# Optimization experiments

Measured on AMD Instinct MI355X. Metric: run time of the kernel, lower is better.

Reference implementation:

```python
import jax, jax.numpy as jnp
import numpy as np

D_MODEL = 1024
NUM_HEADS = 16
ENERGY_SCALE = 0.1
LN_EPS = 1e-5


def layernorm(x, gamma, beta):
    mu = jnp.mean(x, axis=-1, keepdims=True)
    var = jnp.var(x, axis=-1, keepdims=True)
    return (x - mu) * jax.lax.rsqrt(var + LN_EPS) * gamma + beta


def setup_inputs() -> dict:
    key = jax.random.key(0)
    ks = jax.random.split(key, 8)
    B, L, D = 2, 2048, D_MODEL
    s = 0.02
    return {
        "x": jax.random.normal(ks[0], (B, L, D), dtype=jnp.float32),
        "wq": jax.random.normal(ks[1], (D, D), dtype=jnp.float32) * s,
        "wk": jax.random.normal(ks[2], (D, D), dtype=jnp.float32) * s,
        "wv": jax.random.normal(ks[3], (D, D), dtype=jnp.float32) * s,
        "wo_w": jax.random.normal(ks[4], (D, D), dtype=jnp.float32) * s,
        "wo_b": jnp.zeros((D,), dtype=jnp.float32),
        "ep_w": jax.random.normal(ks[5], (D, D), dtype=jnp.float32) * s,
        "ep_b": jnp.zeros((D,), dtype=jnp.float32),
        "en_g": jnp.ones((D,), dtype=jnp.float32),
        "en_b": jnp.zeros((D,), dtype=jnp.float32),
        "ln_g": jnp.ones((D,), dtype=jnp.float32),
        "ln_b": jnp.zeros((D,), dtype=jnp.float32),
    }


def reference(x, wq, wk, wv, wo_w, wo_b, ep_w, ep_b, en_g, en_b, ln_g, ln_b):
    B, L, D = x.shape
    H, dk = NUM_HEADS, D // NUM_HEADS
    # Linear projections (torch convention: y = x @ W^T), split heads -> [B,H,L,dk]
    q = (x @ wq.T).reshape(B, L, H, dk).transpose(0, 2, 1, 3)
    k = (x @ wk.T).reshape(B, L, H, dk).transpose(0, 2, 1, 3)
    v = (x @ wv.T).reshape(B, L, H, dk).transpose(0, 2, 1, 3)
    scores = jnp.einsum("bhld,bhmd->bhlm", q, k) / jnp.sqrt(jnp.float32(dk))
    # Energy bias: ef @ ef^T as a proper GEMM (same math as the broadcast-mul-sum)
    ef = layernorm(x @ ep_w.T + ep_b, en_g, en_b)
    energy_bias = jnp.einsum("bld,bmd->blm", ef, ef)  # [B,L,L]
    scores = scores + ENERGY_SCALE * energy_bias[:, None, :, :]
    attn = jax.nn.softmax(scores, axis=-1)  # dropout is identity in eval mode
    ctx = jnp.einsum("bhlm,bhmd->bhld", attn, v)
    ctx = ctx.transpose(0, 2, 1, 3).reshape(B, L, D)
    out = ctx @ wo_w.T + wo_b
    return layernorm(out + x, ln_g, ln_b), attn
```

## Files before the change

kernel.cpp:

```cpp
#include <hip/hip_runtime.h>
#include <math.h>

#define D_MODEL 1024
#define NUM_HEADS 16
#define DK 64
#define L_SEQ 2048
#define BATCH 2
#define LN_EPS 1e-5f
#define ENERGY_SCALE 0.1f

typedef __attribute__((ext_vector_type(8))) short short8;
typedef __attribute__((ext_vector_type(4))) float f32x4;
typedef __attribute__((address_space(1))) const unsigned int gas_u32;
typedef __attribute__((address_space(3))) unsigned int las_u32;

__device__ __forceinline__ float waveReduceSum(float v) {
#pragma unroll
    for (int off = 32; off > 0; off >>= 1) v += __shfl_xor(v, off, 64);
    return v;
}

__device__ __forceinline__ unsigned short f2bf(float f) {
    unsigned int u = __float_as_uint(f);
    u += 0x7fff + ((u >> 16) & 1);
    return (unsigned short)(u >> 16);
}
__device__ __forceinline__ float bf2f(unsigned short u) {
    return __uint_as_float((unsigned int)u << 16);
}

__global__ __launch_bounds__(256) void cvt6(
    const float* s0, const float* s1, const float* s2,
    const float* s3, const float* s4, const float* s5,
    unsigned short* d0, unsigned short* d1, unsigned short* d2,
    unsigned short* d3, unsigned short* d4, unsigned short* d5,
    long long n0, long long n1, long long n2, long long n3, long long n4, long long n5)
{
    const float* s; unsigned short* d; long long n;
    switch (blockIdx.y) {
        case 0: s = s0; d = d0; n = n0; break;
        case 1: s = s1; d = d1; n = n1; break;
        case 2: s = s2; d = d2; n = n2; break;
        case 3: s = s3; d = d3; n = n3; break;
        case 4: s = s4; d = d4; n = n4; break;
        default: s = s5; d = d5; n = n5; break;
    }
    long long i = ((long long)blockIdx.x * 256 + threadIdx.x) * 4;
    if (i >= n) return;
    float4 v = *(const float4*)(s + i);
    ushort4 o;
    o.x = f2bf(v.x); o.y = f2bf(v.y); o.z = f2bf(v.z); o.w = f2bf(v.w);
    *(ushort4*)(d + i) = o;
}

__global__ __launch_bounds__(256) void gemm_bf16(
    const unsigned short* __restrict__ A, const unsigned short* __restrict__ B,
    const float* __restrict__ bias, float* __restrict__ Cf, unsigned short* __restrict__ Ch,
    int N, int K, long long sA, long long sB, long long sC)
{
    A += (long long)blockIdx.z * sA;
    B += (long long)blockIdx.z * sB;
    __shared__ unsigned short As[128 * 64];
    __shared__ unsigned short Bs[128 * 64];
    const int tid = threadIdx.x;
    const int lane = tid & 63, w = tid >> 6;
    const int quad = lane >> 4, col = lane & 15;
    const int wm = w & 1, wn = w >> 1;
    const int row0 = blockIdx.y * 128, col0 = blockIdx.x * 128;

    const int lr = lane >> 3, lc = lane & 7;
    const int gcs = (lc ^ lr) * 8;

    f32x4 acc[4][4];
#pragma unroll
    for (int mt = 0; mt < 4; mt++)
#pragma unroll
        for (int nt = 0; nt < 4; nt++) acc[mt][nt] = (f32x4){0.f, 0.f, 0.f, 0.f};

    for (int k0 = 0; k0 < K; k0 += 64) {
        __syncthreads();
#pragma unroll
        for (int p = 0; p < 4; p++) {
            const int rb = w * 32 + p * 8;
            __builtin_amdgcn_global_load_lds(
                (gas_u32*)(A + (long long)(row0 + rb + lr) * K + k0 + gcs),
                (las_u32*)(As + rb * 64), 16, 0, 0);
            __builtin_amdgcn_global_load_lds(
                (gas_u32*)(B + (long long)(col0 + rb + lr) * K + k0 + gcs),
                (las_u32*)(Bs + rb * 64), 16, 0, 0);
        }
        __syncthreads();
#pragma unroll
        for (int kc = 0; kc < 2; kc++) {
            const int csw = ((quad + 4 * kc) ^ (col & 7)) * 8;
            short8 af[4], bfr[4];
#pragma unroll
            for (int mt = 0; mt < 4; mt++)
                af[mt] = *(const short8*)(As + (wm * 64 + mt * 16 + col) * 64 + csw);
#pragma unroll
            for (int nt = 0; nt < 4; nt++)
                bfr[nt] = *(const short8*)(Bs + (wn * 64 + nt * 16 + col) * 64 + csw);
#pragma unroll
            for (int mt = 0; mt < 4; mt++)
#pragma unroll
                for (int nt = 0; nt < 4; nt++)
                    acc[mt][nt] = __builtin_amdgcn_mfma_f32_16x16x32_bf16(af[mt], bfr[nt], acc[mt][nt], 0, 0, 0);
        }
    }

#pragma unroll
    for (int mt = 0; mt < 4; mt++)
#pragma unroll
        for (int nt = 0; nt < 4; nt++)
#pragma unroll
            for (int reg = 0; reg < 4; reg++) {
                long long row = row0 + wm * 64 + mt * 16 + quad * 4 + reg;
                int c = col0 + wn * 64 + nt * 16 + col;
                float v = acc[mt][nt][reg];
                if (bias) v += bias[c];
                if (Cf) Cf[blockIdx.z * sC + row * N + c] = v;
                else    Ch[blockIdx.z * sC + row * N + c] = f2bf(v);
            }
}

__global__ __launch_bounds__(256) void proj_gemm(
    const unsigned short* __restrict__ Xh,
    const unsigned short* __restrict__ wqh, const unsigned short* __restrict__ wkh,
    const unsigned short* __restrict__ wvh, const unsigned short* __restrict__ eph,
    const float* __restrict__ ep_b,
    unsigned short* __restrict__ Qh, unsigned short* __restrict__ Kh,
    unsigned short* __restrict__ Vf, float* __restrict__ EP)
{
    const unsigned short* B;
    switch (blockIdx.z) {
        case 0: B = wqh; break;
        case 1: B = wkh; break;
        case 2: B = wvh; break;
        default: B = eph; break;
    }
    __shared__ unsigned short As[128 * 64];
    __shared__ unsigned short Bs[128 * 64];
    const int tid = threadIdx.x;
    const int lane = tid & 63, w = tid >> 6;
    const int quad = lane >> 4, col = lane & 15;
    const int wm = w & 1, wn = w >> 1;
    const int row0 = blockIdx.y * 128, col0 = blockIdx.x * 128;
    const int K = D_MODEL, N = D_MODEL;

    const int lr = lane >> 3, lc = lane & 7;
    const int gcs = (lc ^ lr) * 8;

    f32x4 acc[4][4];
#pragma unroll
    for (int mt = 0; mt < 4; mt++)
#pragma unroll
        for (int nt = 0; nt < 4; nt++) acc[mt][nt] = (f32x4){0.f, 0.f, 0.f, 0.f};

    for (int k0 = 0; k0 < K; k0 += 64) {
        __syncthreads();
#pragma unroll
        for (int p = 0; p < 4; p++) {
            const int rb = w * 32 + p * 8;
            __builtin_amdgcn_global_load_lds(
                (gas_u32*)(Xh + (long long)(row0 + rb + lr) * K + k0 + gcs),
                (las_u32*)(As + rb * 64), 16, 0, 0);
            __builtin_amdgcn_global_load_lds(
                (gas_u32*)(B + (long long)(col0 + rb + lr) * K + k0 + gcs),
                (las_u32*)(Bs + rb * 64), 16, 0, 0);
        }
        __syncthreads();
#pragma unroll
        for (int kc = 0; kc < 2; kc++) {
            const int csw = ((quad + 4 * kc) ^ (col & 7)) * 8;
            short8 af[4], bfr[4];
#pragma unroll
            for (int mt = 0; mt < 4; mt++)
                af[mt] = *(const short8*)(As + (wm * 64 + mt * 16 + col) * 64 + csw);
#pragma unroll
            for (int nt = 0; nt < 4; nt++)
                bfr[nt] = *(const short8*)(Bs + (wn * 64 + nt * 16 + col) * 64 + csw);
#pragma unroll
            for (int mt = 0; mt < 4; mt++)
#pragma unroll
                for (int nt = 0; nt < 4; nt++)
                    acc[mt][nt] = __builtin_amdgcn_mfma_f32_16x16x32_bf16(af[mt], bfr[nt], acc[mt][nt], 0, 0, 0);
        }
    }

    unsigned short* Hout = (blockIdx.z == 0) ? Qh : (blockIdx.z == 1) ? Kh : Vf;
#pragma unroll
    for (int mt = 0; mt < 4; mt++)
#pragma unroll
        for (int nt = 0; nt < 4; nt++)
#pragma unroll
            for (int reg = 0; reg < 4; reg++) {
                long long row = row0 + wm * 64 + mt * 16 + quad * 4 + reg;
                int c = col0 + wn * 64 + nt * 16 + col;
                float v = acc[mt][nt][reg];
                if (blockIdx.z == 3) EP[row * N + c] = v + ep_b[c];
                else                 Hout[row * N + c] = f2bf(v);
            }
}

__global__ __launch_bounds__(256) void ln_rows(
    const float* __restrict__ in, const float* __restrict__ res,
    const float* __restrict__ g, const float* __restrict__ bta,
    float* __restrict__ outf, unsigned short* __restrict__ outh)
{
    const long long row = blockIdx.x;
    const float* ip = in + row * D_MODEL;
    const float* rp = res ? res + row * D_MODEL : nullptr;
    const int tid = threadIdx.x;
    float vals[4];
    float s = 0.f, ss = 0.f;
#pragma unroll
    for (int j = 0; j < 4; j++) {
        int idx = tid + j * 256;
        float v = ip[idx];
        if (rp) v += rp[idx];
        vals[j] = v; s += v; ss += v * v;
    }
    __shared__ float sred[4], ssred[4];
    s = waveReduceSum(s); ss = waveReduceSum(ss);
    int wave = tid >> 6, lane = tid & 63;
    if (lane == 0) { sred[wave] = s; ssred[wave] = ss; }
    __syncthreads();
    float ts = sred[0] + sred[1] + sred[2] + sred[3];
    float tss = ssred[0] + ssred[1] + ssred[2] + ssred[3];
    float mu = ts * (1.f / D_MODEL);
    float var = tss * (1.f / D_MODEL) - mu * mu;
    float rs = rsqrtf(var + LN_EPS);
#pragma unroll
    for (int j = 0; j < 4; j++) {
        int idx = tid + j * 256;
        float o = (vals[j] - mu) * rs * g[idx] + bta[idx];
        if (outf) outf[row * D_MODEL + idx] = o;
        else      outh[row * D_MODEL + idx] = f2bf(o);
    }
}

__global__ __launch_bounds__(256) void transpose_v(
    const unsigned short* __restrict__ V, unsigned short* __restrict__ Vt)
{
    const int m0 = blockIdx.x * 64, h = blockIdx.y, b = blockIdx.z;
    __shared__ unsigned int t[64][65];
    const int tid = threadIdx.x;
    {
        int r = tid >> 4, c4 = (tid & 15) * 4;
#pragma unroll
        for (int i = 0; i < 4; i++) {
            int row = r + i * 16;
            ushort4 v = *(const ushort4*)(V + ((long long)b * L_SEQ + m0 + row) * D_MODEL + h * DK + c4);
            t[row][c4] = v.x; t[row][c4 + 1] = v.y; t[row][c4 + 2] = v.z; t[row][c4 + 3] = v.w;
        }
    }
    __syncthreads();
    const int lane = tid & 63, wv = tid >> 6;
#pragma unroll
    for (int i = 0; i < 16; i++) {
        int d = wv * 16 + i;
        Vt[(((long long)(b * NUM_HEADS + h)) * DK + d) * L_SEQ + m0 + lane] = (unsigned short)t[lane][d];
    }
}

__global__ __launch_bounds__(256) void eb_stats(
    const float* __restrict__ EB, float* __restrict__ ebmax, float* __restrict__ ebtmax)
{
    const long long row = blockIdx.x;
    const float* p = EB + row * L_SEQ;
    const int tid = threadIdx.x;
    float4 a = *(const float4*)(p + tid * 8);
    float4 c = *(const float4*)(p + tid * 8 + 4);
    float m = fmaxf(fmaxf(fmaxf(a.x, a.y), fmaxf(a.z, a.w)),
                    fmaxf(fmaxf(c.x, c.y), fmaxf(c.z, c.w)));
    m = fmaxf(m, __shfl_xor(m, 1, 64));
    m = fmaxf(m, __shfl_xor(m, 2, 64));
    m = fmaxf(m, __shfl_xor(m, 4, 64));
    if ((tid & 7) == 0) ebtmax[row * 32 + (tid >> 3)] = m;
    m = fmaxf(m, __shfl_xor(m, 8, 64));
    m = fmaxf(m, __shfl_xor(m, 16, 64));
    m = fmaxf(m, __shfl_xor(m, 32, 64));
    __shared__ float red[4];
    if ((tid & 63) == 0) red[tid >> 6] = m;
    __syncthreads();
    if (tid == 0)
        ebmax[row] = fmaxf(fmaxf(red[0], red[1]), fmaxf(red[2], red[3]));
}

__global__ __launch_bounds__(256) void qk_stats(
    const unsigned short* __restrict__ Qh, const unsigned short* __restrict__ Kh,
    float* __restrict__ qn, float* __restrict__ kn)
{
    const int l0 = blockIdx.x * 64, h = blockIdx.y, b = blockIdx.z;
    const int tid = threadIdx.x;
    const int r = tid >> 2, p4 = (tid & 3) * 16;
    const unsigned short* q = Qh + ((long long)b * L_SEQ + l0 + r) * D_MODEL + h * DK + p4;
    const unsigned short* k = Kh + ((long long)b * L_SEQ + l0 + r) * D_MODEL + h * DK + p4;
    float sq = 0.f, sk = 0.f;
#pragma unroll
    for (int i = 0; i < 16; i++) {
        float qv = bf2f(q[i]); sq += qv * qv;
        float kv = bf2f(k[i]); sk += kv * kv;
    }
    sq += __shfl_xor(sq, 1, 64); sq += __shfl_xor(sq, 2, 64);
    sk += __shfl_xor(sk, 1, 64); sk += __shfl_xor(sk, 2, 64);
    if ((tid & 3) == 0) {
        long long idx = ((long long)(b * NUM_HEADS + h)) * L_SEQ + l0 + r;
        qn[idx] = sqrtf(sq);
        kn[idx] = sqrtf(sk);
    }
}

__global__ __launch_bounds__(256) void kstats2(
    const float* __restrict__ kn, float* __restrict__ kmax, float* __restrict__ ktmax)
{
    const long long bh = blockIdx.x;
    const float* p = kn + bh * L_SEQ;
    const int tid = threadIdx.x;
    float4 a = *(const float4*)(p + tid * 8);
    float4 c = *(const float4*)(p + tid * 8 + 4);
    float m = fmaxf(fmaxf(fmaxf(a.x, a.y), fmaxf(a.z, a.w)),
                    fmaxf(fmaxf(c.x, c.y), fmaxf(c.z, c.w)));
    m = fmaxf(m, __shfl_xor(m, 1, 64));
    m = fmaxf(m, __shfl_xor(m, 2, 64));
    m = fmaxf(m, __shfl_xor(m, 4, 64));
    if ((tid & 7) == 0) ktmax[bh * 32 + (tid >> 3)] = m;
    m = fmaxf(m, __shfl_xor(m, 8, 64));
    m = fmaxf(m, __shfl_xor(m, 16, 64));
    m = fmaxf(m, __shfl_xor(m, 32, 64));
    __shared__ float red[4];
    if ((tid & 63) == 0) red[tid >> 6] = m;
    __syncthreads();
    if (tid == 0)
        kmax[bh] = fmaxf(fmaxf(red[0], red[1]), fmaxf(red[2], red[3]));
}

__global__ __launch_bounds__(64) void skip_mask(
    const float* __restrict__ ebmax, const float* __restrict__ ebtmax,
    const float* __restrict__ qn, const float* __restrict__ kmax,
    const float* __restrict__ ktmax, unsigned int* __restrict__ skipm)
{
    const int l0 = blockIdx.x * 64, h = blockIdx.y, b = blockIdx.z;
    const int tid = threadIdx.x;
    const int row = l0 + tid;
    const int bh = b * NUM_HEADS + h;
    float q = qn[(long long)bh * L_SEQ + row];
    float Mh = ENERGY_SCALE * ebmax[(long long)b * L_SEQ + row] + q * kmax[bh] * 0.125f + 0.02f;
    const float* ebt = ebtmax + ((long long)b * L_SEQ + row) * 32;
    const float* ktm = ktmax + bh * 32;
    unsigned int m = 0;
    for (int t = 0; t < 32; t++) {
        float ub = ENERGY_SCALE * ebt[t] + q * ktm[t] * 0.125f;
        unsigned long long bal = __ballot(ub < Mh - 45.0f);
        if (bal == ~0ull) m |= (1u << t);
    }
    if (tid == 0) skipm[bh * 32 + blockIdx.x] = m;
}

__global__ __launch_bounds__(256) void attn_mfma(
    const unsigned short* __restrict__ Qh, const unsigned short* __restrict__ Kh,
    const unsigned short* __restrict__ Vt, const float* __restrict__ EB,
    const float* __restrict__ ebmax, const float* __restrict__ qn,
    const float* __restrict__ kmax, const unsigned int* __restrict__ skipm,
    float* __restrict__ attn_out, unsigned short* __restrict__ CTXh)
{
    __shared__ unsigned short Ks[64 * 72];
    __shared__ unsigned short Vts[64 * 72];
    __shared__ unsigned short Ps[4 * 16 * 72];

    const int tid = threadIdx.x;
    const int lane = tid & 63, w = tid >> 6;
    const int quad = lane >> 4, col = lane & 15;
    const int l0 = blockIdx.x * 64;
    const int h = blockIdx.y, b = blockIdx.z;

    const unsigned int sm = skipm[(b * NUM_HEADS + h) * 32 + blockIdx.x];

    {
        float* zbase = attn_out + (((long long)(b * NUM_HEADS + h)) * L_SEQ + l0) * L_SEQ;
        const int zc = (tid & 15) * 4;
        const int zr = tid >> 4;
        const float4 zv = {0.f, 0.f, 0.f, 0.f};
        for (int t = 0; t < 32; t++) {
            if (!(sm & (1u << t))) continue;
            float* tb = zbase + t * 64 + zc;
#pragma unroll
            for (int rr = 0; rr < 4; rr++)
                *(float4*)(tb + (long long)(rr * 16 + zr) * L_SEQ) = zv;
        }
    }

    short8 aq[2];
    {
        const unsigned short* qrow = Qh + ((long long)b * L_SEQ + l0 + w * 16 + col) * D_MODEL + h * DK;
        aq[0] = *(const short8*)(qrow + quad * 8);
        aq[1] = *(const short8*)(qrow + 32 + quad * 8);
    }

    float Mhat[4];
    {
        const float km = kmax[b * NUM_HEADS + h];
#pragma unroll
        for (int reg = 0; reg < 4; reg++) {
            int row = l0 + w * 16 + quad * 4 + reg;
            float qb = qn[((long long)(b * NUM_HEADS + h)) * L_SEQ + row];
            Mhat[reg] = ENERGY_SCALE * ebmax[(long long)b * L_SEQ + row] +
                        qb * km * 0.125f + 0.02f;
        }
    }

    const float* ebp = EB + ((long long)b * L_SEQ + l0 + w * 16 + quad * 4) * L_SEQ + col;
    const unsigned short* kbase = Kh + ((long long)b * L_SEQ) * D_MODEL + h * DK;
    const unsigned short* vbase = Vt + ((long long)(b * NUM_HEADS + h)) * DK * L_SEQ;

    const int sr = tid >> 2, sc0 = (tid & 3) * 16;

    float rowSacc[4] = {0.f, 0.f, 0.f, 0.f};
    for (int t = 0; t < 32; t++) {
        if (sm & (1u << t)) continue;
        const int m0 = t * 64;
        __syncthreads();
        *(uint4*)(Ks + sr * 72 + sc0)     = *(const uint4*)(kbase + (long long)(m0 + sr) * D_MODEL + sc0);
        *(uint4*)(Ks + sr * 72 + sc0 + 8) = *(const uint4*)(kbase + (long long)(m0 + sr) * D_MODEL + sc0 + 8);
        __syncthreads();

        f32x4 acc[4];
#pragma unroll
        for (int nt = 0; nt < 4; nt++) acc[nt] = (f32x4){0.f, 0.f, 0.f, 0.f};
#pragma unroll
        for (int nt = 0; nt < 4; nt++)
#pragma unroll
            for (int kc = 0; kc < 2; kc++) {
                short8 bk = *(const short8*)(Ks + (nt * 16 + col) * 72 + quad * 8 + kc * 32);
                acc[nt] = __builtin_amdgcn_mfma_f32_16x16x32_bf16(aq[kc], bk, acc[nt], 0, 0, 0);
            }
#pragma unroll
        for (int nt = 0; nt < 4; nt++)
#pragma unroll
            for (int reg = 0; reg < 4; reg++) {
                float s = acc[nt][reg] * 0.125f + ENERGY_SCALE * ebp[(long long)reg * L_SEQ + m0 + nt * 16];
                rowSacc[reg] += __expf(s - Mhat[reg]);
            }
    }

    float invS[4];
#pragma unroll
    for (int reg = 0; reg < 4; reg++) {
        float v = rowSacc[reg];
#pragma unroll
        for (int off = 8; off > 0; off >>= 1) v += __shfl_xor(v, off, 64);
        invS[reg] = 1.f / v;
    }

    f32x4 ctx[4];
#pragma unroll
    for (int nt = 0; nt < 4; nt++) ctx[nt] = (f32x4){0.f, 0.f, 0.f, 0.f};

    unsigned short* Psw = Ps + w * 16 * 72;
    float* aob = attn_out + (((long long)(b * NUM_HEADS + h)) * L_SEQ + l0 + w * 16 + quad * 4) * L_SEQ + col;

    for (int t = 0; t < 32; t++) {
        if (sm & (1u << t)) continue;
        const int m0 = t * 64;
        __syncthreads();
        *(uint4*)(Ks + sr * 72 + sc0)      = *(const uint4*)(kbase + (long long)(m0 + sr) * D_MODEL + sc0);
        *(uint4*)(Ks + sr * 72 + sc0 + 8)  = *(const uint4*)(kbase + (long long)(m0 + sr) * D_MODEL + sc0 + 8);
        *(uint4*)(Vts + sr * 72 + sc0)     = *(const uint4*)(vbase + (long long)sr * L_SEQ + m0 + sc0);
        *(uint4*)(Vts + sr * 72 + sc0 + 8) = *(const uint4*)(vbase + (long long)sr * L_SEQ + m0 + sc0 + 8);
        __syncthreads();

        f32x4 acc[4];
#pragma unroll
        for (int nt = 0; nt < 4; nt++) acc[nt] = (f32x4){0.f, 0.f, 0.f, 0.f};
#pragma unroll
        for (int nt = 0; nt < 4; nt++)
#pragma unroll
            for (int kc = 0; kc < 2; kc++) {
                short8 bk = *(const short8*)(Ks + (nt * 16 + col) * 72 + quad * 8 + kc * 32);
                acc[nt] = __builtin_amdgcn_mfma_f32_16x16x32_bf16(aq[kc], bk, acc[nt], 0, 0, 0);
            }

#pragma unroll
        for (int nt = 0; nt < 4; nt++)
#pragma unroll
            for (int reg = 0; reg < 4; reg++) {
                float s = acc[nt][reg] * 0.125f + ENERGY_SCALE * ebp[(long long)reg * L_SEQ + m0 + nt * 16];
                float p = __expf(s - Mhat[reg]) * invS[reg];
                aob[(long long)reg * L_SEQ + m0 + nt * 16] = p;
                Psw[(quad * 4 + reg) * 72 + nt * 16 + col] = f2bf(p);
            }

        short8 ap[2];
#pragma unroll
        for (int kc = 0; kc < 2; kc++)
            ap[kc] = *(const short8*)(Psw + col * 72 + quad * 8 + kc * 32);
#pragma unroll
        for (int nt = 0; nt < 4; nt++)
#pragma unroll
            for (int kc = 0; kc < 2; kc++) {
                short8 bv = *(const short8*)(Vts + (nt * 16 + col) * 72 + quad * 8 + kc * 32);
                ctx[nt] = __builtin_amdgcn_mfma_f32_16x16x32_bf16(ap[kc], bv, ctx[nt], 0, 0, 0);
            }
    }

#pragma unroll
    for (int nt = 0; nt < 4; nt++)
#pragma unroll
        for (int reg = 0; reg < 4; reg++)
            CTXh[((long long)b * L_SEQ + l0 + w * 16 + quad * 4 + reg) * D_MODEL + h * DK + nt * 16 + col] =
                f2bf(ctx[nt][reg]);
}

extern "C" void kernel_launch(void* const* d_in, const int* in_sizes, int n_in,
                              void* d_out, int out_size, void* d_ws, size_t ws_size,
                              hipStream_t stream) {
    const float* x    = (const float*)d_in[0];
    const float* wq   = (const float*)d_in[1];
    const float* wk   = (const float*)d_in[2];
    const float* wv   = (const float*)d_in[3];
    const float* wo_w = (const float*)d_in[4];
    const float* wo_b = (const float*)d_in[5];
    const float* ep_w = (const float*)d_in[6];
    const float* ep_b = (const float*)d_in[7];
    const float* en_g = (const float*)d_in[8];
    const float* en_b = (const float*)d_in[9];
    const float* ln_g = (const float*)d_in[10];
    const float* ln_b = (const float*)d_in[11];

    float* out_final = (float*)d_out;
    float* attn_out  = out_final + (long long)BATCH * L_SEQ * D_MODEL;

    const long long MD = (long long)BATCH * L_SEQ * D_MODEL;
    const long long WN = (long long)D_MODEL * D_MODEL;
    const long long BH = (long long)BATCH * NUM_HEADS;

    float* EB = (float*)d_ws;
    float* EP = EB + (long long)BATCH * L_SEQ * L_SEQ;
    unsigned short* Xh   = (unsigned short*)(EP + MD);
    unsigned short* Qh   = Xh + MD;
    unsigned short* Kh   = Qh + MD;
    unsigned short* Vf   = Kh + MD;
    unsigned short* Vt   = Vf + MD;
    unsigned short* EFh  = Vt + MD;
    unsigned short* CTXh = EFh + MD;
    unsigned short* wqh  = CTXh + MD;
    unsigned short* wkh  = wqh + WN;
    unsigned short* wvh  = wkh + WN;
    unsigned short* eph  = wvh + WN;
    unsigned short* woh  = eph + WN;
    float* ebmax  = (float*)(woh + WN);
    float* qn     = ebmax + (long long)BATCH * L_SEQ;
    float* kn     = qn + BH * L_SEQ;
    float* kmax   = kn + BH * L_SEQ;
    float* ktmax  = kmax + BH;
    float* ebtmax = ktmax + BH * 32;
    unsigned int* skipm = (unsigned int*)(ebtmax + (long long)BATCH * L_SEQ * 32);
    float* OUT = EP;

    const int M = BATCH * L_SEQ;
    dim3 blk(256);

    cvt6<<<dim3((unsigned)(MD / 1024), 6), blk, 0, stream>>>(
        x, wq, wk, wv, ep_w, wo_w, Xh, wqh, wkh, wvh, eph, woh,
        MD, WN, WN, WN, WN, WN);

    proj_gemm<<<dim3(D_MODEL / 128, M / 128, 4), blk, 0, stream>>>(
        Xh, wqh, wkh, wvh, eph, ep_b, Qh, Kh, Vf, EP);

    ln_rows<<<dim3(M), blk, 0, stream>>>(EP, nullptr, en_g, en_b, nullptr, EFh);

    gemm_bf16<<<dim3(L_SEQ / 128, L_SEQ / 128, BATCH), blk, 0, stream>>>(
        EFh, EFh, nullptr, EB, nullptr, L_SEQ, D_MODEL,
        (long long)L_SEQ * D_MODEL, (long long)L_SEQ * D_MODEL,
        (long long)L_SEQ * L_SEQ);

    qk_stats<<<dim3(L_SEQ / 64, NUM_HEADS, BATCH), blk, 0, stream>>>(Qh, Kh, qn, kn);
    kstats2<<<dim3((unsigned)BH), blk, 0, stream>>>(kn, kmax, ktmax);
    eb_stats<<<dim3(M), blk, 0, stream>>>(EB, ebmax, ebtmax);
    skip_mask<<<dim3(L_SEQ / 64, NUM_HEADS, BATCH), dim3(64), 0, stream>>>(
        ebmax, ebtmax, qn, kmax, ktmax, skipm);

    transpose_v<<<dim3(L_SEQ / 64, NUM_HEADS, BATCH), blk, 0, stream>>>(Vf, Vt);

    attn_mfma<<<dim3(L_SEQ / 64, NUM_HEADS, BATCH), blk, 0, stream>>>(
        Qh, Kh, Vt, EB, ebmax, qn, kmax, skipm, attn_out, CTXh);

    gemm_bf16<<<dim3(D_MODEL / 128, M / 128, 1), blk, 0, stream>>>(
        CTXh, woh, wo_b, OUT, nullptr, D_MODEL, D_MODEL, 0, 0, 0);

    ln_rows<<<dim3(M), blk, 0, stream>>>(OUT, x, ln_g, ln_b, out_final, nullptr);
}
```

Measured before the change: 758.5 us.

## Double-buffer K tiles via async global_load_lds with XOR-swizzled LDS layout

Replaces the register-staged K/V tile loads in both attention passes with direct global-to-LDS async loads. K tiles are double-buffered so the next non-skipped tile is prefetched during compute. The LDS layout switches from padded rows to an XOR swizzle to avoid bank conflicts, and s_setprio is placed around the MFMA blocks. The barrier structure is reworked, which adds risk around synchronization: the V tile is loaded and consumed within the same iteration, relying on the mid-iteration barrier.

```diff
diff --git a/kernel.cpp b/kernel.cpp
--- a/kernel.cpp
+++ b/kernel.cpp
@@ -364,8 +364,8 @@
     const float* __restrict__ kmax, const unsigned int* __restrict__ skipm,
     float* __restrict__ attn_out, unsigned short* __restrict__ CTXh)
 {
-    __shared__ unsigned short Ks[64 * 72];
-    __shared__ unsigned short Vts[64 * 72];
+    __shared__ unsigned short Ks[2][64 * 64];
+    __shared__ unsigned short Vts[64 * 64];
     __shared__ unsigned short Ps[4 * 16 * 72];
 
     const int tid = threadIdx.x;
@@ -375,6 +375,29 @@
     const int h = blockIdx.y, b = blockIdx.z;
 
     const unsigned int sm = skipm[(b * NUM_HEADS + h) * 32 + blockIdx.x];
+
+    const unsigned short* kbase = Kh + ((long long)b * L_SEQ) * D_MODEL + h * DK;
+    const unsigned short* vbase = Vt + ((long long)(b * NUM_HEADS + h)) * DK * L_SEQ;
+
+    const int lr = lane >> 3, lc = lane & 7;
+    const int gsw = (lc ^ lr) * 8;
+
+    auto nxt = [&](int t) -> int {
+        unsigned int rem = ~sm;
+        if (t >= 0) rem &= (t >= 31) ? 0u : (0xFFFFFFFFu << (t + 1));
+        return rem ? (int)__builtin_ctz(rem) : -1;
+    };
+    const int t0 = nxt(-1);
+
+    if (t0 >= 0) {
+#pragma unroll
+        for (int p = 0; p < 2; p++) {
+            const int rb = w * 8 + p * 32;
+            __builtin_amdgcn_global_load_lds(
+                (gas_u32*)(kbase + (long long)(t0 * 64 + rb + lr) * D_MODEL + gsw),
+                (las_u32*)(&Ks[0][rb * 64]), 16, 0, 0);
+        }
+    }
 
     {
         float* zbase = attn_out + (((long long)(b * NUM_HEADS + h)) * L_SEQ + l0) * L_SEQ;
@@ -410,30 +433,37 @@
     }
 
     const float* ebp = EB + ((long long)b * L_SEQ + l0 + w * 16 + quad * 4) * L_SEQ + col;
-    const unsigned short* kbase = Kh + ((long long)b * L_SEQ) * D_MODEL + h * DK;
-    const unsigned short* vbase = Vt + ((long long)(b * NUM_HEADS + h)) * DK * L_SEQ;
-
-    const int sr = tid >> 2, sc0 = (tid & 3) * 16;
+
+    __syncthreads();
 
     float rowSacc[4] = {0.f, 0.f, 0.f, 0.f};
-    for (int t = 0; t < 32; t++) {
-        if (sm & (1u << t)) continue;
+    int cur = 0;
+    for (int t = t0; t >= 0; ) {
+        const int tn = nxt(t);
+        if (tn >= 0) {
+#pragma unroll
+            for (int p = 0; p < 2; p++) {
+                const int rb = w * 8 + p * 32;
+                __builtin_amdgcn_global_load_lds(
+                    (gas_u32*)(kbase + (long long)(tn * 64 + rb + lr) * D_MODEL + gsw),
+                    (las_u32*)(&Ks[cur ^ 1][rb * 64]), 16, 0, 0);
+            }
+        }
         const int m0 = t * 64;
-        __syncthreads();
-        *(uint4*)(Ks + sr * 72 + sc0)     = *(const uint4*)(kbase + (long long)(m0 + sr) * D_MODEL + sc0);
-        *(uint4*)(Ks + sr * 72 + sc0 + 8) = *(const uint4*)(kbase + (long long)(m0 + sr) * D_MODEL + sc0 + 8);
-        __syncthreads();
 
         f32x4 acc[4];
 #pragma unroll
         for (int nt = 0; nt < 4; nt++) acc[nt] = (f32x4){0.f, 0.f, 0.f, 0.f};
+        __builtin_amdgcn_s_setprio(1);
 #pragma unroll
         for (int nt = 0; nt < 4; nt++)
 #pragma unroll
             for (int kc = 0; kc < 2; kc++) {
-                short8 bk = *(const short8*)(Ks + (nt * 16 + col) * 72 + quad * 8 + kc * 32);
+                short8 bk = *(const short8*)(&Ks[cur][((nt * 16 + col) << 6) +
+                                                     (((quad + 4 * kc) ^ (col & 7)) << 3)]);
                 acc[nt] = __builtin_amdgcn_mfma_f32_16x16x32_bf16(aq[kc], bk, acc[nt], 0, 0, 0);
             }
+        __builtin_amdgcn_s_setprio(0);
 #pragma unroll
         for (int nt = 0; nt < 4; nt++)
 #pragma unroll
@@ -441,6 +471,9 @@
                 float s = acc[nt][reg] * 0.125f + ENERGY_SCALE * ebp[(long long)reg * L_SEQ + m0 + nt * 16];
                 rowSacc[reg] += __expf(s - Mhat[reg]);
             }
+        __syncthreads();
+        cur ^= 1;
+        t = tn;
     }
 
     float invS[4];
@@ -452,6 +485,18 @@
         invS[reg] = 1.f / v;
     }
 
+    cur = 0;
+    if (t0 >= 0) {
+#pragma unroll
+        for (int p = 0; p < 2; p++) {
+            const int rb = w * 8 + p * 32;
+            __builtin_amdgcn_global_load_lds(
+                (gas_u32*)(kbase + (long long)(t0 * 64 + rb + lr) * D_MODEL + gsw),
+                (las_u32*)(&Ks[0][rb * 64]), 16, 0, 0);
+        }
+    }
+    __syncthreads();
+
     f32x4 ctx[4];
 #pragma unroll
     for (int nt = 0; nt < 4; nt++) ctx[nt] = (f32x4){0.f, 0.f, 0.f, 0.f};
@@ -459,26 +504,40 @@
     unsigned short* Psw = Ps + w * 16 * 72;
     float* aob = attn_out + (((long long)(b * NUM_HEADS + h)) * L_SEQ + l0 + w * 16 + quad * 4) * L_SEQ + col;
 
-    for (int t = 0; t < 32; t++) {
-        if (sm & (1u << t)) continue;
+    for (int t = t0; t >= 0; ) {
+        const int tn = nxt(t);
         const int m0 = t * 64;
-        __syncthreads();
-        *(uint4*)(Ks + sr * 72 + sc0)      = *(const uint4*)(kbase + (long long)(m0 + sr) * D_MODEL + sc0);
-        *(uint4*)(Ks + sr * 72 + sc0 + 8)  = *(const uint4*)(kbase + (long long)(m0 + sr) * D_MODEL + sc0 + 8);
-        *(uint4*)(Vts + sr * 72 + sc0)     = *(const uint4*)(vbase + (long long)sr * L_SEQ + m0 + sc0);
-        *(uint4*)(Vts + sr * 72 + sc0 + 8) = *(const uint4*)(vbase + (long long)sr * L_SEQ + m0 + sc0 + 8);
-        __syncthreads();
+
+#pragma unroll
+        for (int p = 0; p < 2; p++) {
+            const int rb = w * 8 + p * 32;
+            __builtin_amdgcn_global_load_lds(
+                (gas_u32*)(vbase + (long long)(rb + lr) * L_SEQ + m0 + gsw),
+                (las_u32*)(&Vts[rb * 64]), 16, 0, 0);
+        }
+        if (tn >= 0) {
+#pragma unroll
+            for (int p = 0; p < 2; p++) {
+                const int rb = w * 8 + p * 32;
+                __builtin_amdgcn_global_load_lds(
+                    (gas_u32*)(kbase + (long long)(tn * 64 + rb + lr) * D_MODEL + gsw),
+                    (las_u32*)(&Ks[cur ^ 1][rb * 64]), 16, 0, 0);
+            }
+        }
 
         f32x4 acc[4];
 #pragma unroll
         for (int nt = 0; nt < 4; nt++) acc[nt] = (f32x4){0.f, 0.f, 0.f, 0.f};
+        __builtin_amdgcn_s_setprio(1);
 #pragma unroll
         for (int nt = 0; nt < 4; nt++)
 #pragma unroll
             for (int kc = 0; kc < 2; kc++) {
-                short8 bk = *(const short8*)(Ks + (nt * 16 + col) * 72 + quad * 8 + kc * 32);
+                short8 bk = *(const short8*)(&Ks[cur][((nt * 16 + col) << 6) +
+                                                     (((quad + 4 * kc) ^ (col & 7)) << 3)]);
                 acc[nt] = __builtin_amdgcn_mfma_f32_16x16x32_bf16(aq[kc], bk, acc[nt], 0, 0, 0);
             }
+        __builtin_amdgcn_s_setprio(0);
 
 #pragma unroll
         for (int nt = 0; nt < 4; nt++)
@@ -486,21 +545,34 @@
             for (int reg = 0; reg < 4; reg++) {
                 float s = acc[nt][reg] * 0.125f + ENERGY_SCALE * ebp[(long long)reg * L_SEQ + m0 + nt * 16];
                 float p = __expf(s - Mhat[reg]) * invS[reg];
-                aob[(long long)reg * L_SEQ + m0 + nt * 16] = p;
+                acc[nt][reg] = p;
                 Psw[(quad * 4 + reg) * 72 + nt * 16 + col] = f2bf(p);
             }
+        __syncthreads();
+
+#pragma unroll
+        for (int nt = 0; nt < 4; nt++)
+#pragma unroll
+            for (int reg = 0; reg < 4; reg++)
+                aob[(long long)reg * L_SEQ + m0 + nt * 16] = acc[nt][reg];
 
         short8 ap[2];
 #pragma unroll
         for (int kc = 0; kc < 2; kc++)
             ap[kc] = *(const short8*)(Psw + col * 72 + quad * 8 + kc * 32);
+        __builtin_amdgcn_s_setprio(1);
 #pragma unroll
         for (int nt = 0; nt < 4; nt++)
 #pragma unroll
             for (int kc = 0; kc < 2; kc++) {
-                short8 bv = *(const short8*)(Vts + (nt * 16 + col) * 72 + quad * 8 + kc * 32);
+                short8 bv = *(const short8*)(&Vts[((nt * 16 + col) << 6) +
+                                                  (((quad + 4 * kc) ^ (col & 7)) << 3)]);
                 ctx[nt] = __builtin_amdgcn_mfma_f32_16x16x32_bf16(ap[kc], bv, ctx[nt], 0, 0, 0);
             }
+        __builtin_amdgcn_s_setprio(0);
+        __syncthreads();
+        cur ^= 1;
+        t = tn;
     }
 
 #pragma unroll
```

Result: no change. 752.8 us (-0.7%).
